# Optimization experiments

Measured on AMD Instinct MI355X. Metric: run time of the kernel, lower is better.

The kernel has to match this reference:

```python
import jax, jax.numpy as jnp
import numpy as np

B, T, I, H = 128, 512, 256, 512  # batch, seq_len, num_encoder_tokens, latent_dim


def setup_inputs() -> dict:
    key = jax.random.key(0)
    k0, k1, k2, k3, k4 = jax.random.split(key, 5)
    s = 1.0 / np.sqrt(H).astype(np.float32)  # PyTorch GRU init: U(-1/sqrt(H), 1/sqrt(H))
    return {
        "encoder_inputs": jax.random.normal(k0, (B, T, I), dtype=jnp.float32),
        "W_ih": jax.random.uniform(k1, (3 * H, I), jnp.float32, -s, s),
        "W_hh": jax.random.uniform(k2, (3 * H, H), jnp.float32, -s, s),
        "b_ih": jax.random.uniform(k3, (3 * H,), jnp.float32, -s, s),
        "b_hh": jax.random.uniform(k4, (3 * H,), jnp.float32, -s, s),
    }


def _gru_final_state(encoder_inputs, W_ih, W_hh, b_ih, b_hh):
    # Precompute input projections for all timesteps in one big GEMM: [B,T,3H]
    x_gates = jnp.einsum('bti,gi->btg', encoder_inputs, W_ih) + b_ih
    x_gates = jnp.swapaxes(x_gates, 0, 1)  # [T,B,3H] for scan over time
    Hdim = W_hh.shape[1]
    h0 = jnp.zeros((encoder_inputs.shape[0], Hdim), encoder_inputs.dtype)

    def step(h, xg):
        hg = h @ W_hh.T + b_hh                      # [B,3H]
        xr, xz, xn = jnp.split(xg, 3, axis=-1)      # PyTorch gate order: r, z, n
        hr, hz, hn = jnp.split(hg, 3, axis=-1)
        r = jax.nn.sigmoid(xr + hr)
        z = jax.nn.sigmoid(xz + hz)
        n = jnp.tanh(xn + r * hn)
        h_new = (1.0 - z) * n + z * h
        return h_new, None

    h_final, _ = jax.lax.scan(step, h0, x_gates)
    return h_final[None]  # [num_layers=1, B, H], matching torch's state_h


def reference(encoder_inputs, W_ih, W_hh, b_ih, b_hh):
    return _gru_final_state(encoder_inputs, W_ih, W_hh, b_ih, b_hh)
```

## Files before the change

kernel.cpp:

```cpp
#include <hip/hip_runtime.h>
#include <hip/hip_bf16.h>

#define BB   128
#define TT   512
#define II   256
#define HH   512
#define G3   1536

typedef __attribute__((ext_vector_type(8))) short short8;
typedef __attribute__((ext_vector_type(4))) float f32x4;
typedef __attribute__((ext_vector_type(4))) unsigned int u32x4;

__device__ __forceinline__ float bf2f(unsigned short u) {
    union { unsigned int u; float f; } p; p.u = ((unsigned int)u) << 16; return p.f;
}
__device__ __forceinline__ unsigned short f2bf(float f) {
    union { float f; unsigned int u; } p; p.f = f;
    unsigned int r = p.u + 0x7fffu + ((p.u >> 16) & 1u);
    return (unsigned short)(r >> 16);
}
__device__ __forceinline__ float sigmoidf_fast(float x) {
    return 1.0f / (1.0f + __expf(-x));
}
__device__ __forceinline__ float tanhf_fast(float x) {
    return 1.0f - 2.0f / (1.0f + __expf(2.0f * x));
}

#define GLD16O(dst, base, OFFSTR)                                         \
    asm volatile("global_load_dwordx4 %0, %1, off offset:" OFFSTR " sc0 sc1" \
                 : "=v"(dst) : "v"(base))

__global__ __launch_bounds__(256) void xgate_gemm(
    const float* __restrict__ x,
    const float* __restrict__ Wih,
    const float* __restrict__ bih,
    unsigned short* __restrict__ xg)
{
    __shared__ unsigned short AS[128][40];
    __shared__ unsigned short BS[128][40];

    const int t   = blockIdx.y;
    const int g0  = blockIdx.x * 128;
    const int tid = threadIdx.x;
    const int lane = tid & 63;
    const int w    = tid >> 6;
    const int wr   = w >> 1, wc = w & 1;

    f32x4 acc[4][4];
#pragma unroll
    for (int a = 0; a < 4; ++a)
#pragma unroll
        for (int b = 0; b < 4; ++b) acc[a][b] = (f32x4)(0.0f);

    for (int kk = 0; kk < 8; ++kk) {
        const int k0 = kk * 32;
#pragma unroll
        for (int ii = 0; ii < 4; ++ii) {
            int slot = tid + 256 * ii;
            int row  = slot >> 3;
            int c4   = slot & 7;
            float4 av = *(const float4*)(x + ((size_t)row * TT + t) * II + k0 + c4 * 4);
            unsigned short* ap = &AS[row][c4 * 4];
            ap[0] = f2bf(av.x); ap[1] = f2bf(av.y); ap[2] = f2bf(av.z); ap[3] = f2bf(av.w);
            float4 bv = *(const float4*)(Wih + (size_t)(g0 + row) * II + k0 + c4 * 4);
            unsigned short* bp = &BS[row][c4 * 4];
            bp[0] = f2bf(bv.x); bp[1] = f2bf(bv.y); bp[2] = f2bf(bv.z); bp[3] = f2bf(bv.w);
        }
        __syncthreads();

        const int kc = (lane >> 4) * 8;
        short8 a[4], b[4];
#pragma unroll
        for (int mi = 0; mi < 4; ++mi)
            a[mi] = *(const short8*)&AS[wr * 64 + mi * 16 + (lane & 15)][kc];
#pragma unroll
        for (int ni = 0; ni < 4; ++ni)
            b[ni] = *(const short8*)&BS[wc * 64 + ni * 16 + (lane & 15)][kc];
#pragma unroll
        for (int mi = 0; mi < 4; ++mi)
#pragma unroll
            for (int ni = 0; ni < 4; ++ni)
                acc[mi][ni] = __builtin_amdgcn_mfma_f32_16x16x32_bf16(a[mi], b[ni], acc[mi][ni], 0, 0, 0);
        __syncthreads();
    }

#pragma unroll
    for (int ni = 0; ni < 4; ++ni) {
        const int col = wc * 64 + ni * 16 + (lane & 15);
        const float bias = bih[g0 + col];
#pragma unroll
        for (int mi = 0; mi < 4; ++mi) {
#pragma unroll
            for (int i = 0; i < 4; ++i) {
                const int row = wr * 64 + mi * 16 + (lane >> 4) * 4 + i;
                xg[((size_t)t * BB + row) * G3 + g0 + col] = f2bf(acc[mi][ni][i] + bias);
            }
        }
    }
}

#define NTH2 128

__global__ __launch_bounds__(NTH2, 1) void gru_scan(
    const unsigned short* __restrict__ xg,
    const float* __restrict__ Whh,
    const float* __restrict__ bhh,
    float* __restrict__ out,
    unsigned long long* __restrict__ hb64)
{
    __shared__ unsigned int hF[2 * 4096];

    const int g    = blockIdx.x & 7;
    const int m    = blockIdx.x >> 3;
    const int tid  = threadIdx.x;
    const int lane = tid & 63;
    const int w    = tid >> 6;

    const int jj = m * 32 + w * 16 + (lane & 15);
    short8 Wr[3][16];
    {
        const int kofs = (lane >> 4) * 8;
#pragma unroll
        for (int q = 0; q < 3; ++q) {
            const float* wrow = Whh + ((size_t)(q * HH + jj)) * HH + kofs;
#pragma unroll
            for (int ks = 0; ks < 16; ++ks) {
                float4 v0 = *(const float4*)(wrow + ks * 32);
                float4 v1 = *(const float4*)(wrow + ks * 32 + 4);
                union { short8 s; unsigned int u[4]; } pk;
                pk.u[0] = (unsigned int)f2bf(v0.x) | ((unsigned int)f2bf(v0.y) << 16);
                pk.u[1] = (unsigned int)f2bf(v0.z) | ((unsigned int)f2bf(v0.w) << 16);
                pk.u[2] = (unsigned int)f2bf(v1.x) | ((unsigned int)f2bf(v1.y) << 16);
                pk.u[3] = (unsigned int)f2bf(v1.z) | ((unsigned int)f2bf(v1.w) << 16);
                Wr[q][ks] = pk.s;
            }
        }
    }

    const float bhr = bhh[jj];
    const float bhz = bhh[HH + jj];
    const float bhn = bhh[2 * HH + jj];
    const int b0 = (lane >> 4) * 4;

    float hh[4] = {0.0f, 0.0f, 0.0f, 0.0f};

    const int prow = tid & 15;
    const int plg  = (tid >> 4) & 3;
    const int pe2  = tid >> 6;
    const char* pollb = (const char*)hb64 +
        (((size_t)g * 16 + prow) * 256 + plg * 4 + pe2 * 2) * 8;
    const size_t PARITY_B = (size_t)BB * 256 * 8;
    const int dstb = plg * 64 + prow * 4 + pe2 * 2;

    const unsigned int* xg32 = (const unsigned int*)xg;
    const unsigned int xsel = (unsigned int)(jj & 1) * 16;
    unsigned int xoff[12];
#pragma unroll
    for (int i = 0; i < 4; ++i)
#pragma unroll
        for (int q = 0; q < 3; ++q)
            xoff[i * 3 + q] = (unsigned int)(((g * 16 + b0 + i) * G3 + q * HH + (jj & ~1)) >> 1);
    const unsigned int XSTEP = (unsigned int)((BB * G3) >> 1);

    unsigned int xc[12];
#pragma unroll
    for (int v = 0; v < 12; ++v) xc[v] = xg32[xoff[v]];

    for (int t = 0; t < TT; ++t) {
        const unsigned int want = (unsigned int)t;
        const char* pb = pollb + (size_t)(t & 1) * PARITY_B;
        u32x4 P[16];
        while (true) {
            GLD16O(P[ 0], pb, "0");    GLD16O(P[ 1], pb, "128");
            GLD16O(P[ 2], pb, "256");  GLD16O(P[ 3], pb, "384");
            GLD16O(P[ 4], pb, "512");  GLD16O(P[ 5], pb, "640");
            GLD16O(P[ 6], pb, "768");  GLD16O(P[ 7], pb, "896");
            GLD16O(P[ 8], pb, "1024"); GLD16O(P[ 9], pb, "1152");
            GLD16O(P[10], pb, "1280"); GLD16O(P[11], pb, "1408");
            GLD16O(P[12], pb, "1536"); GLD16O(P[13], pb, "1664");
            GLD16O(P[14], pb, "1792"); GLD16O(P[15], pb, "1920");
            asm volatile("s_waitcnt vmcnt(0)" ::: "memory");
            __builtin_amdgcn_sched_barrier(0);
            bool ok = true;
#pragma unroll
            for (int ks = 0; ks < 16; ++ks)
                ok &= (P[ks][1] == want) & (P[ks][3] == want);
            if (ok) break;
        }

        unsigned int* hD = &hF[(t & 1) * 4096 + dstb];
#pragma unroll
        for (int ks = 0; ks < 16; ++ks) {
            unsigned long long dv = (unsigned long long)P[ks][0] |
                                    ((unsigned long long)P[ks][2] << 32);
            *(unsigned long long*)&hD[ks * 256] = dv;
        }

        unsigned int xn[12];
        {
            const unsigned int tw = (t < TT - 1 ? (unsigned int)(t + 1) : (unsigned int)t) * XSTEP;
#pragma unroll
            for (int v = 0; v < 12; ++v) xn[v] = xg32[xoff[v] + tw];
        }

        __syncthreads();

        const char* hA = (const char*)hF + (t & 1) * 16384 + lane * 16;
        f32x4 aR = (f32x4)(0.0f), aZ = (f32x4)(0.0f), aN = (f32x4)(0.0f);
#pragma unroll
        for (int ks = 0; ks < 16; ++ks) {
            short8 a = *(const short8*)(hA + ks * 1024);
            aR = __builtin_amdgcn_mfma_f32_16x16x32_bf16(a, Wr[0][ks], aR, 0, 0, 0);
            aZ = __builtin_amdgcn_mfma_f32_16x16x32_bf16(a, Wr[1][ks], aZ, 0, 0, 0);
            aN = __builtin_amdgcn_mfma_f32_16x16x32_bf16(a, Wr[2][ks], aN, 0, 0, 0);
        }

        const unsigned long long tag = ((unsigned long long)(t + 1)) << 32;
        unsigned long long* dst = hb64 + (size_t)((t + 1) & 1) * BB * 256;
#pragma unroll
        for (int i = 0; i < 4; ++i) {
            float xr = bf2f((unsigned short)(xc[i * 3 + 0] >> xsel));
            float xz = bf2f((unsigned short)(xc[i * 3 + 1] >> xsel));
            float xn_ = bf2f((unsigned short)(xc[i * 3 + 2] >> xsel));
            float r = sigmoidf_fast(xr + aR[i] + bhr);
            float z = sigmoidf_fast(xz + aZ[i] + bhz);
            float n = tanhf_fast(xn_ + r * (aN[i] + bhn));
            hh[i] = (1.0f - z) * n + z * hh[i];
            unsigned int u  = (unsigned int)f2bf(hh[i]);
            unsigned int pv = (unsigned int)__shfl_xor((int)u, 1);
            if ((lane & 1) == 0) {
                unsigned long long word = tag | (unsigned long long)(u | (pv << 16));
                __hip_atomic_store(&dst[(size_t)(g * 16 + b0 + i) * 256 + (jj >> 1)], word,
                                   __ATOMIC_RELAXED, __HIP_MEMORY_SCOPE_AGENT);
            }
        }

#pragma unroll
        for (int v = 0; v < 12; ++v) xc[v] = xn[v];
    }

#pragma unroll
    for (int i = 0; i < 4; ++i)
        out[(size_t)(g * 16 + b0 + i) * HH + jj] = hh[i];
}

extern "C" void kernel_launch(void* const* d_in, const int* in_sizes, int n_in,
                              void* d_out, int out_size, void* d_ws, size_t ws_size,
                              hipStream_t stream) {
    const float* x   = (const float*)d_in[0];
    const float* Wih = (const float*)d_in[1];
    const float* Whh = (const float*)d_in[2];
    const float* bih = (const float*)d_in[3];
    const float* bhh = (const float*)d_in[4];
    float* out = (float*)d_out;

    const size_t XG_BYTES   = (size_t)TT * BB * G3 * 2;
    unsigned short* xg      = (unsigned short*)d_ws;
    unsigned long long* hb64 = (unsigned long long*)((char*)d_ws + XG_BYTES);
    const size_t HBUF_BYTES = (size_t)2 * BB * 256 * 8;

    hipMemsetAsync((char*)d_ws + XG_BYTES, 0, HBUF_BYTES, stream);

    dim3 g1(G3 / 128, TT);
    xgate_gemm<<<g1, 256, 0, stream>>>(x, Wih, bih, xg);

    gru_scan<<<128, NTH2, 0, stream>>>(xg, Whh, bhh, out, hb64);
}
```

Baseline: 1.820 ms.

## Halve scan workgroups by doubling waves per block and split polling across waves

The recurrent GRU scan now launches 64 workgroups of 256 threads instead of 128 of 128, so each block owns 64 hidden columns across 4 waves. Each thread polls half as many hidden-state words, and a wave-wide __all check decides when a step's data is ready. The time loop is manually unrolled by two to remove the parity and x-gate register swaps, and the next-step x-gate loads move after the barrier. The aim is to reduce cross-block synchronization traffic and per-step polling latency, with fewer producers per step, at the cost of more waves contending per CU.

```diff
diff --git a/kernel.cpp b/kernel.cpp
--- a/kernel.cpp
+++ b/kernel.cpp
@@ -99,7 +99,7 @@
     }
 }
 
-#define NTH2 128
+#define NTH2 256
 
 __global__ __launch_bounds__(NTH2, 1) void gru_scan(
     const unsigned short* __restrict__ xg,
@@ -116,7 +116,7 @@
     const int lane = tid & 63;
     const int w    = tid >> 6;
 
-    const int jj = m * 32 + w * 16 + (lane & 15);
+    const int jj = m * 64 + w * 16 + (lane & 15);
     short8 Wr[3][16];
     {
         const int kofs = (lane >> 4) * 8;
@@ -145,12 +145,13 @@
     float hh[4] = {0.0f, 0.0f, 0.0f, 0.0f};
 
     const int prow = tid & 15;
-    const int plg  = (tid >> 4) & 3;
-    const int pe2  = tid >> 6;
+    const int pe2p = (tid >> 4) & 1;
+    const int pksh = (tid >> 5) & 1;
+    const int plg  = tid >> 6;
     const char* pollb = (const char*)hb64 +
-        (((size_t)g * 16 + prow) * 256 + plg * 4 + pe2 * 2) * 8;
+        (((size_t)g * 16 + prow) * 256 + pksh * 128 + plg * 4 + pe2p * 2) * 8;
     const size_t PARITY_B = (size_t)BB * 256 * 8;
-    const int dstb = plg * 64 + prow * 4 + pe2 * 2;
+    const int dstb = pksh * 2048 + plg * 64 + prow * 4 + pe2p * 2;
 
     const unsigned int* xg32 = (const unsigned int*)xg;
     const unsigned int xsel = (unsigned int)(jj & 1) * 16;
@@ -162,82 +163,78 @@
             xoff[i * 3 + q] = (unsigned int)(((g * 16 + b0 + i) * G3 + q * HH + (jj & ~1)) >> 1);
     const unsigned int XSTEP = (unsigned int)((BB * G3) >> 1);
 
-    unsigned int xc[12];
-#pragma unroll
-    for (int v = 0; v < 12; ++v) xc[v] = xg32[xoff[v]];
-
-    for (int t = 0; t < TT; ++t) {
-        const unsigned int want = (unsigned int)t;
-        const char* pb = pollb + (size_t)(t & 1) * PARITY_B;
-        u32x4 P[16];
-        while (true) {
-            GLD16O(P[ 0], pb, "0");    GLD16O(P[ 1], pb, "128");
-            GLD16O(P[ 2], pb, "256");  GLD16O(P[ 3], pb, "384");
-            GLD16O(P[ 4], pb, "512");  GLD16O(P[ 5], pb, "640");
-            GLD16O(P[ 6], pb, "768");  GLD16O(P[ 7], pb, "896");
-            GLD16O(P[ 8], pb, "1024"); GLD16O(P[ 9], pb, "1152");
-            GLD16O(P[10], pb, "1280"); GLD16O(P[11], pb, "1408");
-            GLD16O(P[12], pb, "1536"); GLD16O(P[13], pb, "1664");
-            GLD16O(P[14], pb, "1792"); GLD16O(P[15], pb, "1920");
-            asm volatile("s_waitcnt vmcnt(0)" ::: "memory");
-            __builtin_amdgcn_sched_barrier(0);
-            bool ok = true;
-#pragma unroll
-            for (int ks = 0; ks < 16; ++ks)
-                ok &= (P[ks][1] == want) & (P[ks][3] == want);
-            if (ok) break;
-        }
-
-        unsigned int* hD = &hF[(t & 1) * 4096 + dstb];
-#pragma unroll
-        for (int ks = 0; ks < 16; ++ks) {
-            unsigned long long dv = (unsigned long long)P[ks][0] |
-                                    ((unsigned long long)P[ks][2] << 32);
-            *(unsigned long long*)&hD[ks * 256] = dv;
-        }
-
-        unsigned int xn[12];
-        {
-            const unsigned int tw = (t < TT - 1 ? (unsigned int)(t + 1) : (unsigned int)t) * XSTEP;
-#pragma unroll
-            for (int v = 0; v < 12; ++v) xn[v] = xg32[xoff[v] + tw];
-        }
-
-        __syncthreads();
-
-        const char* hA = (const char*)hF + (t & 1) * 16384 + lane * 16;
-        f32x4 aR = (f32x4)(0.0f), aZ = (f32x4)(0.0f), aN = (f32x4)(0.0f);
-#pragma unroll
-        for (int ks = 0; ks < 16; ++ks) {
-            short8 a = *(const short8*)(hA + ks * 1024);
-            aR = __builtin_amdgcn_mfma_f32_16x16x32_bf16(a, Wr[0][ks], aR, 0, 0, 0);
-            aZ = __builtin_amdgcn_mfma_f32_16x16x32_bf16(a, Wr[1][ks], aZ, 0, 0, 0);
-            aN = __builtin_amdgcn_mfma_f32_16x16x32_bf16(a, Wr[2][ks], aN, 0, 0, 0);
-        }
-
-        const unsigned long long tag = ((unsigned long long)(t + 1)) << 32;
-        unsigned long long* dst = hb64 + (size_t)((t + 1) & 1) * BB * 256;
-#pragma unroll
-        for (int i = 0; i < 4; ++i) {
-            float xr = bf2f((unsigned short)(xc[i * 3 + 0] >> xsel));
-            float xz = bf2f((unsigned short)(xc[i * 3 + 1] >> xsel));
-            float xn_ = bf2f((unsigned short)(xc[i * 3 + 2] >> xsel));
-            float r = sigmoidf_fast(xr + aR[i] + bhr);
-            float z = sigmoidf_fast(xz + aZ[i] + bhz);
-            float n = tanhf_fast(xn_ + r * (aN[i] + bhn));
-            hh[i] = (1.0f - z) * n + z * hh[i];
-            unsigned int u  = (unsigned int)f2bf(hh[i]);
-            unsigned int pv = (unsigned int)__shfl_xor((int)u, 1);
-            if ((lane & 1) == 0) {
-                unsigned long long word = tag | (unsigned long long)(u | (pv << 16));
-                __hip_atomic_store(&dst[(size_t)(g * 16 + b0 + i) * 256 + (jj >> 1)], word,
-                                   __ATOMIC_RELAXED, __HIP_MEMORY_SCOPE_AGENT);
-            }
-        }
-
-#pragma unroll
-        for (int v = 0; v < 12; ++v) xc[v] = xn[v];
-    }
+    unsigned int xcA[12], xcB[12];
+#pragma unroll
+    for (int v = 0; v < 12; ++v) xcA[v] = xg32[xoff[v]];
+
+#define STEP(T, PAR, XC, XN)                                                   \
+    {                                                                          \
+        const unsigned int want = (unsigned int)(T);                           \
+        const char* pb = pollb + (size_t)(PAR) * PARITY_B;                     \
+        u32x4 P[8];                                                            \
+        while (true) {                                                         \
+            GLD16O(P[0], pb, "0");   GLD16O(P[1], pb, "128");                  \
+            GLD16O(P[2], pb, "256"); GLD16O(P[3], pb, "384");                  \
+            GLD16O(P[4], pb, "512"); GLD16O(P[5], pb, "640");                  \
+            GLD16O(P[6], pb, "768"); GLD16O(P[7], pb, "896");                  \
+            asm volatile("s_waitcnt vmcnt(0)" ::: "memory");                   \
+            __builtin_amdgcn_sched_barrier(0);                                 \
+            bool ok = true;                                                    \
+            _Pragma("unroll")                                                  \
+            for (int j = 0; j < 8; ++j)                                        \
+                ok &= (P[j][1] == want) & (P[j][3] == want);                   \
+            if (__all(ok)) break;                                              \
+        }                                                                      \
+        unsigned int* hD = &hF[(PAR) * 4096 + dstb];                           \
+        _Pragma("unroll")                                                      \
+        for (int j = 0; j < 8; ++j) {                                          \
+            unsigned long long dv = (unsigned long long)P[j][0] |              \
+                                    ((unsigned long long)P[j][2] << 32);       \
+            *(unsigned long long*)&hD[j * 256] = dv;                           \
+        }                                                                      \
+        __syncthreads();                                                       \
+        {           \
+            const unsigned int tw =                                            \
+                ((T) < TT - 1 ? (unsigned int)(T) + 1u : (unsigned int)(T)) * XSTEP; \
+            _Pragma("unroll")                                                  \
+            for (int v = 0; v < 12; ++v) XN[v] = xg32[xoff[v] + tw];           \
+        }                                                                      \
+        const char* hA = (const char*)hF + (PAR) * 16384 + lane * 16;          \
+        f32x4 aR = (f32x4)(0.0f), aZ = (f32x4)(0.0f), aN = (f32x4)(0.0f);      \
+        _Pragma("unroll")                                                      \
+        for (int ks = 0; ks < 16; ++ks) {                                      \
+            short8 a = *(const short8*)(hA + ks * 1024);                       \
+            aR = __builtin_amdgcn_mfma_f32_16x16x32_bf16(a, Wr[0][ks], aR, 0, 0, 0); \
+            aZ = __builtin_amdgcn_mfma_f32_16x16x32_bf16(a, Wr[1][ks], aZ, 0, 0, 0); \
+            aN = __builtin_amdgcn_mfma_f32_16x16x32_bf16(a, Wr[2][ks], aN, 0, 0, 0); \
+        }                                                                      \
+        const unsigned long long tag = ((unsigned long long)((T) + 1)) << 32;  \
+        unsigned long long* dst = hb64 + (size_t)(((T) + 1) & 1) * BB * 256;   \
+        _Pragma("unroll")                                                      \
+        for (int i = 0; i < 4; ++i) {                                          \
+            float xr  = bf2f((unsigned short)(XC[i * 3 + 0] >> xsel));         \
+            float xz  = bf2f((unsigned short)(XC[i * 3 + 1] >> xsel));         \
+            float xnv = bf2f((unsigned short)(XC[i * 3 + 2] >> xsel));         \
+            float r = sigmoidf_fast(xr + aR[i] + bhr);                         \
+            float z = sigmoidf_fast(xz + aZ[i] + bhz);                         \
+            float n = tanhf_fast(xnv + r * (aN[i] + bhn));                     \
+            hh[i] = (1.0f - z) * n + z * hh[i];                                \
+            unsigned int u  = (unsigned int)f2bf(hh[i]);                       \
+            unsigned int pv = (unsigned int)__shfl_xor((int)u, 1);             \
+            if ((lane & 1) == 0) {                                             \
+                unsigned long long word = tag | (unsigned long long)(u | (pv << 16)); \
+                __hip_atomic_store(&dst[(size_t)(g * 16 + b0 + i) * 256 + (jj >> 1)], \
+                                   word, __ATOMIC_RELAXED, __HIP_MEMORY_SCOPE_AGENT); \
+            }                                                                  \
+        }                                                                      \
+    }
+
+    for (int s = 0; s < TT / 2; ++s) {
+        const int t0 = 2 * s;
+        STEP(t0,     0, xcA, xcB);
+        STEP(t0 + 1, 1, xcB, xcA);
+    }
+#undef STEP
 
 #pragma unroll
     for (int i = 0; i < 4; ++i)
@@ -264,5 +261,5 @@
     dim3 g1(G3 / 128, TT);
     xgate_gemm<<<g1, 256, 0, stream>>>(x, Wih, bih, xg);
 
-    gru_scan<<<128, NTH2, 0, stream>>>(xg, Whh, bhh, out, hb64);
-}
+    gru_scan<<<64, NTH2, 0, stream>>>(xg, Whh, bhh, out, hb64);
+}
```

Result: slower. 2.667 ms (+46.5%).

## Use 32 wider scan blocks with split cooperative polling of hidden state

Applied to the files above, without the earlier changes.

The recurrent scan kernel now runs as 32 blocks of 512 threads instead of 128 blocks of 128 threads, so each block covers 128 hidden units. Polling of the published hidden-state words is split across the eight waves: each thread reads four 16-byte chunks instead of sixteen, and readiness is checked with a wave-wide vote before the LDS store and a raw barrier. The input-gate loads are no longer prefetched one step ahead; they are issued after polling. This cuts per-thread polling traffic and the number of cross-block participants, but shortens the window for hiding the gate-load latency.

```diff
diff --git a/kernel.cpp b/kernel.cpp
--- a/kernel.cpp
+++ b/kernel.cpp
@@ -99,7 +99,7 @@
     }
 }
 
-#define NTH2 128
+#define NTH2 512
 
 __global__ __launch_bounds__(NTH2, 1) void gru_scan(
     const unsigned short* __restrict__ xg,
@@ -116,7 +116,7 @@
     const int lane = tid & 63;
     const int w    = tid >> 6;
 
-    const int jj = m * 32 + w * 16 + (lane & 15);
+    const int jj = m * 128 + w * 16 + (lane & 15);
     short8 Wr[3][16];
     {
         const int kofs = (lane >> 4) * 8;
@@ -146,11 +146,11 @@
 
     const int prow = tid & 15;
     const int plg  = (tid >> 4) & 3;
-    const int pe2  = tid >> 6;
+    const int pksh = tid >> 6;
     const char* pollb = (const char*)hb64 +
-        (((size_t)g * 16 + prow) * 256 + plg * 4 + pe2 * 2) * 8;
+        ((size_t)g * 16 + prow) * 2048 + pksh * 256 + plg * 32;
     const size_t PARITY_B = (size_t)BB * 256 * 8;
-    const int dstb = plg * 64 + prow * 4 + pe2 * 2;
+    const int dstbyte = pksh * 2048 + plg * 256 + prow * 16;
 
     const unsigned int* xg32 = (const unsigned int*)xg;
     const unsigned int xsel = (unsigned int)(jj & 1) * 16;
@@ -162,48 +162,38 @@
             xoff[i * 3 + q] = (unsigned int)(((g * 16 + b0 + i) * G3 + q * HH + (jj & ~1)) >> 1);
     const unsigned int XSTEP = (unsigned int)((BB * G3) >> 1);
 
-    unsigned int xc[12];
-#pragma unroll
-    for (int v = 0; v < 12; ++v) xc[v] = xg32[xoff[v]];
+    const unsigned int* xgp = xg32;
 
     for (int t = 0; t < TT; ++t) {
         const unsigned int want = (unsigned int)t;
         const char* pb = pollb + (size_t)(t & 1) * PARITY_B;
-        u32x4 P[16];
+        u32x4 Pa0, Pa1, Pb0, Pb1;
         while (true) {
-            GLD16O(P[ 0], pb, "0");    GLD16O(P[ 1], pb, "128");
-            GLD16O(P[ 2], pb, "256");  GLD16O(P[ 3], pb, "384");
-            GLD16O(P[ 4], pb, "512");  GLD16O(P[ 5], pb, "640");
-            GLD16O(P[ 6], pb, "768");  GLD16O(P[ 7], pb, "896");
-            GLD16O(P[ 8], pb, "1024"); GLD16O(P[ 9], pb, "1152");
-            GLD16O(P[10], pb, "1280"); GLD16O(P[11], pb, "1408");
-            GLD16O(P[12], pb, "1536"); GLD16O(P[13], pb, "1664");
-            GLD16O(P[14], pb, "1792"); GLD16O(P[15], pb, "1920");
+            GLD16O(Pa0, pb, "0");   GLD16O(Pa1, pb, "16");
+            GLD16O(Pb0, pb, "128"); GLD16O(Pb1, pb, "144");
             asm volatile("s_waitcnt vmcnt(0)" ::: "memory");
             __builtin_amdgcn_sched_barrier(0);
-            bool ok = true;
-#pragma unroll
-            for (int ks = 0; ks < 16; ++ks)
-                ok &= (P[ks][1] == want) & (P[ks][3] == want);
-            if (ok) break;
-        }
-
-        unsigned int* hD = &hF[(t & 1) * 4096 + dstb];
-#pragma unroll
-        for (int ks = 0; ks < 16; ++ks) {
-            unsigned long long dv = (unsigned long long)P[ks][0] |
-                                    ((unsigned long long)P[ks][2] << 32);
-            *(unsigned long long*)&hD[ks * 256] = dv;
-        }
-
-        unsigned int xn[12];
+            bool ok = (Pa0[1] == want) & (Pa0[3] == want) &
+                      (Pa1[1] == want) & (Pa1[3] == want) &
+                      (Pb0[1] == want) & (Pb0[3] == want) &
+                      (Pb1[1] == want) & (Pb1[3] == want);
+            if (__all(ok)) break;
+        }
+
+        unsigned int xc[12];
+#pragma unroll
+        for (int v = 0; v < 12; ++v) xc[v] = xgp[xoff[v]];
+
         {
-            const unsigned int tw = (t < TT - 1 ? (unsigned int)(t + 1) : (unsigned int)t) * XSTEP;
-#pragma unroll
-            for (int v = 0; v < 12; ++v) xn[v] = xg32[xoff[v] + tw];
-        }
-
-        __syncthreads();
+            char* hD = (char*)hF + (t & 1) * 16384 + dstbyte;
+            u32x4 A; A[0] = Pa0[0]; A[1] = Pa0[2]; A[2] = Pa1[0]; A[3] = Pa1[2];
+            *(u32x4*)hD = A;
+            u32x4 B; B[0] = Pb0[0]; B[1] = Pb0[2]; B[2] = Pb1[0]; B[3] = Pb1[2];
+            *(u32x4*)(hD + 1024) = B;
+        }
+
+        asm volatile("s_waitcnt lgkmcnt(0)" ::: "memory");
+        __builtin_amdgcn_s_barrier();
 
         const char* hA = (const char*)hF + (t & 1) * 16384 + lane * 16;
         f32x4 aR = (f32x4)(0.0f), aZ = (f32x4)(0.0f), aN = (f32x4)(0.0f);
@@ -219,12 +209,12 @@
         unsigned long long* dst = hb64 + (size_t)((t + 1) & 1) * BB * 256;
 #pragma unroll
         for (int i = 0; i < 4; ++i) {
-            float xr = bf2f((unsigned short)(xc[i * 3 + 0] >> xsel));
-            float xz = bf2f((unsigned short)(xc[i * 3 + 1] >> xsel));
-            float xn_ = bf2f((unsigned short)(xc[i * 3 + 2] >> xsel));
+            float xr  = bf2f((unsigned short)(xc[i * 3 + 0] >> xsel));
+            float xz  = bf2f((unsigned short)(xc[i * 3 + 1] >> xsel));
+            float xnv = bf2f((unsigned short)(xc[i * 3 + 2] >> xsel));
             float r = sigmoidf_fast(xr + aR[i] + bhr);
             float z = sigmoidf_fast(xz + aZ[i] + bhz);
-            float n = tanhf_fast(xn_ + r * (aN[i] + bhn));
+            float n = tanhf_fast(xnv + r * (aN[i] + bhn));
             hh[i] = (1.0f - z) * n + z * hh[i];
             unsigned int u  = (unsigned int)f2bf(hh[i]);
             unsigned int pv = (unsigned int)__shfl_xor((int)u, 1);
@@ -235,8 +225,7 @@
             }
         }
 
-#pragma unroll
-        for (int v = 0; v < 12; ++v) xc[v] = xn[v];
+        xgp += XSTEP;
     }
 
 #pragma unroll
@@ -255,14 +244,14 @@
     float* out = (float*)d_out;
 
     const size_t XG_BYTES   = (size_t)TT * BB * G3 * 2;
-    unsigned short* xg      = (unsigned short*)d_ws;
+    unsigned short* xg       = (unsigned short*)d_ws;
     unsigned long long* hb64 = (unsigned long long*)((char*)d_ws + XG_BYTES);
-    const size_t HBUF_BYTES = (size_t)2 * BB * 256 * 8;
-
-    hipMemsetAsync((char*)d_ws + XG_BYTES, 0, HBUF_BYTES, stream);
+    const size_t HB_BYTES   = (size_t)2 * BB * 256 * 8;
+
+    hipMemsetAsync((char*)d_ws + XG_BYTES, 0, HB_BYTES, stream);
 
     dim3 g1(G3 / 128, TT);
     xgate_gemm<<<g1, 256, 0, stream>>>(x, Wih, bih, xg);
 
-    gru_scan<<<128, NTH2, 0, stream>>>(xg, Whh, bhh, out, hb64);
-}
+    gru_scan<<<32, NTH2, 0, stream>>>(xg, Whh, bhh, out, hb64);
+}
```

Measured after the change: 2.832 ms. 1.56x slower.
